# Kernel optimization log

Hardware: AMD Instinct MI355X
Metric: run time of the kernel (lower is better)

Reference implementation:

```python
import jax, jax.numpy as jnp
import numpy as np

D_MODEL = 1024
D_STATE = 16
EXPAND = 2
D_INNER = D_MODEL * EXPAND
BATCH = 512
SEQ = 100
DT = 0.01


def setup_inputs() -> dict:
    key = jax.random.key(0)
    ks = jax.random.split(key, 12)
    s = 0.02
    log_ts = jnp.linspace(jnp.log(0.001), jnp.log(0.1), D_STATE).reshape(1, D_STATE)
    return {
        "x": jax.random.normal(ks[0], (BATCH, SEQ, D_MODEL), jnp.float32),
        "pos_emb": jax.random.normal(ks[1], (1, 100, D_MODEL), jnp.float32),
        "W_in": jax.random.normal(ks[2], (D_INNER, D_MODEL), jnp.float32) * s,
        "b_in": jnp.zeros((D_INNER,), jnp.float32),
        "W_gate": jax.random.normal(ks[3], (D_INNER, D_MODEL), jnp.float32) * s,
        "b_gate": jnp.zeros((D_INNER,), jnp.float32),
        "A_log": log_ts.astype(jnp.float32),
        "W_B": jax.random.normal(ks[4], (D_STATE, D_INNER), jnp.float32) * s,
        "b_B": jnp.zeros((D_STATE,), jnp.float32),
        "W_C": jax.random.normal(ks[5], (D_STATE, D_MODEL), jnp.float32) * s,
        "b_C": jnp.zeros((D_STATE,), jnp.float32),
        "W_out": jax.random.normal(ks[6], (D_MODEL, D_INNER), jnp.float32) * s,
        "b_out": jnp.zeros((D_MODEL,), jnp.float32),
    }


def reference(x, pos_emb, W_in, b_in, W_gate, b_gate, A_log, W_B, b_B, W_C, b_C, W_out, b_out):
    b, s, _ = x.shape
    d_inner = W_in.shape[0]
    d_state = A_log.shape[-1]
    x = x + pos_emb[:, :s, :]
    x_proj = jnp.einsum("bsd,id->bsi", x, W_in) + b_in
    gate = jax.nn.sigmoid(jnp.einsum("bsd,id->bsi", x, W_gate) + b_gate)
    x_gated = x_proj * gate
    B = jnp.einsum("bsi,ni->bsn", x_gated, W_B) + b_B   # (b, s, d_state)
    C = jnp.einsum("bsd,nd->bsn", x, W_C) + b_C         # (b, s, d_state)
    A = jnp.exp(DT * jnp.exp(A_log))                      # (1, d_state), broadcasts over batch

    def step(h, bc):
        Bt, Ct = bc
        h = A * h + Bt
        return h, h * Ct

    h0 = jnp.zeros((b, d_state), x.dtype)
    _, ys = jax.lax.scan(step, h0, (jnp.swapaxes(B, 0, 1), jnp.swapaxes(C, 0, 1)))
    y = jnp.swapaxes(ys, 0, 1)                            # (b, s, d_state)
    d_slice = min(d_state, d_inner)
    expanded = jnp.pad(y[:, :, :d_slice], ((0, 0), (0, 0), (0, d_inner - d_slice)))
    return jnp.einsum("bsi,di->bsd", expanded, W_out) + b_out
```

## Files before the change

### kernel.cpp

```cpp
#include <hip/hip_runtime.h>
#include <hip/hip_bf16.h>
#include <stdint.h>

typedef unsigned short u16;
typedef u16   u16x8 __attribute__((ext_vector_type(8)));
typedef short s16x8 __attribute__((ext_vector_type(8)));
typedef float f32x4 __attribute__((ext_vector_type(4)));

#define TOKENS 51200
#define DMODEL 1024
#define DINNER 2048
#define NSTATE 16
#define SEQLEN 100

#define OFF_XP    0ull
#define OFF_WCAT  104857600ull
#define OFF_WB    113246208ull
#define OFF_WC    113311744ull
#define OFF_BPART 113344512ull
#define OFF_BFIN  165773312ull
#define OFF_CBUF  169050112ull
#define OFF_Y     172326912ull

__device__ __forceinline__ u16 f2b(float f) {
  uint32_t u = __float_as_uint(f);
  uint32_t r = (u + 0x7fffu + ((u >> 16) & 1u)) >> 16;
  return (u16)r;
}
__device__ __forceinline__ float b2f(u16 u) {
  return __uint_as_float(((uint32_t)u) << 16);
}

#define GLL(gp, lp) __builtin_amdgcn_global_load_lds( \
    (__attribute__((address_space(1))) unsigned int*)(gp), \
    (__attribute__((address_space(3))) unsigned int*)(lp), 16, 0, 0)
#define SB0() __builtin_amdgcn_sched_barrier(0)

__global__ void k_prep_x(const float* __restrict__ x, const float* __restrict__ pos,
                         u16* __restrict__ xp) {
  long e = ((long)blockIdx.x * blockDim.x + threadIdx.x) * 8;
  int d = (int)(e & (DMODEL - 1));
  long tok = e >> 10;
  int s = (int)(tok % SEQLEN);
  f32x4 a0 = *(const f32x4*)(x + e);
  f32x4 a1 = *(const f32x4*)(x + e + 4);
  f32x4 p0 = *(const f32x4*)(pos + (size_t)s * DMODEL + d);
  f32x4 p1 = *(const f32x4*)(pos + (size_t)s * DMODEL + d + 4);
  u16x8 o;
  o[0] = f2b(a0[0] + p0[0]); o[1] = f2b(a0[1] + p0[1]);
  o[2] = f2b(a0[2] + p0[2]); o[3] = f2b(a0[3] + p0[3]);
  o[4] = f2b(a1[0] + p1[0]); o[5] = f2b(a1[1] + p1[1]);
  o[6] = f2b(a1[2] + p1[2]); o[7] = f2b(a1[3] + p1[3]);
  *(u16x8*)(xp + e) = o;
}

__global__ void k_prep_w(const float* __restrict__ Win, const float* __restrict__ Wg,
                         u16* __restrict__ w2) {
  long e = ((long)blockIdx.x * blockDim.x + threadIdx.x) * 8;
  int r = (int)(e >> 10), c = (int)(e & 1023);
  int srow = ((r >> 5) << 4) + (r & 15);
  const float* src = ((r & 16) ? Wg : Win) + (size_t)srow * DMODEL + c;
  f32x4 a0 = *(const f32x4*)src;
  f32x4 a1 = *(const f32x4*)(src + 4);
  u16x8 o;
  o[0] = f2b(a0[0]); o[1] = f2b(a0[1]); o[2] = f2b(a0[2]); o[3] = f2b(a0[3]);
  o[4] = f2b(a1[0]); o[5] = f2b(a1[1]); o[6] = f2b(a1[2]); o[7] = f2b(a1[3]);
  *(u16x8*)(w2 + e) = o;
}

__global__ void k_prep_wbc(const float* __restrict__ WB, const float* __restrict__ WC,
                           u16* __restrict__ wb, u16* __restrict__ wc) {
  long e = ((long)blockIdx.x * blockDim.x + threadIdx.x) * 8;
  const float* src; u16* dst;
  if (e < 32768) { src = WB + e; dst = wb + e; }
  else           { src = WC + (e - 32768); dst = wc + (e - 32768); }
  f32x4 a0 = *(const f32x4*)src;
  f32x4 a1 = *(const f32x4*)(src + 4);
  u16x8 o;
  o[0] = f2b(a0[0]); o[1] = f2b(a0[1]); o[2] = f2b(a0[2]); o[3] = f2b(a0[3]);
  o[4] = f2b(a1[0]); o[5] = f2b(a1[1]); o[6] = f2b(a1[2]); o[7] = f2b(a1[3]);
  *(u16x8*)(dst) = o;
}

__global__ __launch_bounds__(512, 2) void k_gemm256(
    const u16* __restrict__ XP, const u16* __restrict__ W2, const u16* __restrict__ WBb,
    const float* __restrict__ b_in, const float* __restrict__ b_gate,
    float* __restrict__ Bpart) {
  extern __shared__ __align__(16) u16 smem[];
  char* smemc = (char*)smem;

  const int tid = threadIdx.x;
  const int bid = blockIdx.x;
  const int nb = ((bid & 7) << 1) | ((bid >> 3) & 1);
  const int rb = bid >> 4;
  const int m0 = rb << 8;
  const int n0 = nb << 8;

  const int arow  = tid >> 3;
  const int acolsw = ((tid & 7) ^ (arow & 7)) << 3;
  const u16* gA = XP + (size_t)(m0 + arow) * DMODEL + acolsw;
  const u16* gB = W2 + (size_t)(n0 + arow) * DMODEL + acolsw;
  const int ldst = tid << 3;

  const int wid = tid >> 6, lane = tid & 63;
  const int wm = wid >> 2, wn = wid & 3;
  const int l15 = lane & 15, lhi = lane >> 4;
  const int swz = (l15 & 7) << 4;
  const int arow0 = (wm << 7) + l15;
  const int brow0 = (wn << 6) + l15;

  auto rdA = [&](int bufb, int m, int ks) -> s16x8 {
    return *(const s16x8*)(smemc + bufb + ((arow0 + (m << 4)) << 7) +
                           (((ks << 6) + (lhi << 4)) ^ swz));
  };
  auto rdB = [&](int bufb, int n, int ks) -> s16x8 {
    return *(const s16x8*)(smemc + bufb + 32768 + ((brow0 + (n << 4)) << 7) +
                           (((ks << 6) + (lhi << 4)) ^ swz));
  };
  auto stgA = [&](int t, int i) {
    const int bb = (t & 1) << 15;
    const size_t go = (size_t)t << 6;
    GLL(gA + go + ((size_t)(2 * i)     << 16), smem + bb + ((2 * i)     << 12) + ldst);
    GLL(gA + go + ((size_t)(2 * i + 1) << 16), smem + bb + ((2 * i + 1) << 12) + ldst);
  };
  auto stgB = [&](int t, int i) {
    const int bb = (t & 1) << 15;
    const size_t go = (size_t)t << 6;
    GLL(gB + go + ((size_t)(2 * i)     << 16), smem + bb + 16384 + ((2 * i)     << 12) + ldst);
    GLL(gB + go + ((size_t)(2 * i + 1) << 16), smem + bb + 16384 + ((2 * i + 1) << 12) + ldst);
  };

  f32x4 acc[8][4] = {};

  stgA(0, 0); stgA(0, 1); stgB(0, 0); stgB(0, 1);
  stgA(1, 0); stgA(1, 1); stgB(1, 0); stgB(1, 1);

#pragma unroll 1
  for (int t = 0; t < 16; ++t) {
    if (t == 15) asm volatile("s_waitcnt vmcnt(0)" ::: "memory");
    else         asm volatile("s_waitcnt vmcnt(8)" ::: "memory");
    SB0();
    asm volatile("s_barrier" ::: "memory");
    SB0();
    const int bufb = (t & 1) << 16;

    s16x8 afl[4][2], afh[4][2], bfr[4][2];
#pragma unroll
    for (int m = 0; m < 4; ++m) { afl[m][0] = rdA(bufb, m, 0); afl[m][1] = rdA(bufb, m, 1); }
#pragma unroll
    for (int n = 0; n < 2; ++n) { bfr[n][0] = rdB(bufb, n, 0); bfr[n][1] = rdB(bufb, n, 1); }
    __builtin_amdgcn_s_setprio(1);
#pragma unroll
    for (int ks = 0; ks < 2; ++ks)
#pragma unroll
      for (int m = 0; m < 4; ++m)
#pragma unroll
        for (int n = 0; n < 2; ++n)
          acc[m][n] = __builtin_amdgcn_mfma_f32_16x16x32_bf16(afl[m][ks], bfr[n][ks], acc[m][n], 0, 0, 0);
    __builtin_amdgcn_s_setprio(0);

#pragma unroll
    for (int n = 2; n < 4; ++n) { bfr[n][0] = rdB(bufb, n, 0); bfr[n][1] = rdB(bufb, n, 1); }
    __builtin_amdgcn_s_setprio(1);
#pragma unroll
    for (int ks = 0; ks < 2; ++ks)
#pragma unroll
      for (int m = 0; m < 4; ++m)
#pragma unroll
        for (int n = 0; n < 2; ++n)
          acc[m][n + 2] = __builtin_amdgcn_mfma_f32_16x16x32_bf16(afl[m][ks], bfr[n + 2][ks], acc[m][n + 2], 0, 0, 0);
    __builtin_amdgcn_s_setprio(0);

#pragma unroll
    for (int m = 0; m < 4; ++m) { afh[m][0] = rdA(bufb, m + 4, 0); afh[m][1] = rdA(bufb, m + 4, 1); }
    asm volatile("s_waitcnt lgkmcnt(0)" ::: "memory");
    SB0();
    asm volatile("s_barrier" ::: "memory");
    SB0();

    if (t < 14) stgA(t + 2, 0);
    SB0();
    __builtin_amdgcn_s_setprio(1);
#pragma unroll
    for (int ks = 0; ks < 2; ++ks)
#pragma unroll
      for (int m = 0; m < 4; ++m)
#pragma unroll
        for (int n = 0; n < 2; ++n)
          acc[m + 4][n + 2] = __builtin_amdgcn_mfma_f32_16x16x32_bf16(afh[m][ks], bfr[n + 2][ks], acc[m + 4][n + 2], 0, 0, 0);
    __builtin_amdgcn_s_setprio(0);
    SB0();
    if (t < 14) stgA(t + 2, 1);
    SB0();
    __builtin_amdgcn_s_setprio(1);
#pragma unroll
    for (int m = 0; m < 4; ++m)
#pragma unroll
      for (int n = 0; n < 2; ++n)
        acc[m + 4][n] = __builtin_amdgcn_mfma_f32_16x16x32_bf16(afh[m][0], bfr[n][0], acc[m + 4][n], 0, 0, 0);
    __builtin_amdgcn_s_setprio(0);
    SB0();
    if (t < 14) stgB(t + 2, 0);
    SB0();
    __builtin_amdgcn_s_setprio(1);
#pragma unroll
    for (int m = 0; m < 4; ++m)
#pragma unroll
      for (int n = 0; n < 2; ++n)
        acc[m + 4][n] = __builtin_amdgcn_mfma_f32_16x16x32_bf16(afh[m][1], bfr[n][1], acc[m + 4][n], 0, 0, 0);
    __builtin_amdgcn_s_setprio(0);
    SB0();
    if (t < 14) stgB(t + 2, 1);
    SB0();
  }

  asm volatile("s_waitcnt lgkmcnt(0)" ::: "memory");
  SB0();
  asm volatile("s_barrier" ::: "memory");
  SB0();

  u16* xg = smem;
  float bi[2], bg[2];
#pragma unroll
  for (int u = 0; u < 2; ++u) {
    const int gcol = (nb << 7) + (((wn << 1) + u) << 4) + l15;
    bi[u] = b_in[gcol];
    bg[u] = b_gate[gcol];
  }
#pragma unroll
  for (int m = 0; m < 8; ++m)
#pragma unroll
    for (int u = 0; u < 2; ++u)
#pragma unroll
      for (int j = 0; j < 4; ++j) {
        const int row = (wm << 7) + (m << 4) + (lhi << 2) + j;
        const int col = (((wn << 1) + u) << 4) + l15;
        float pv = acc[m][2 * u][j] + bi[u];
        float gv = acc[m][2 * u + 1][j] + bg[u];
        xg[row * 136 + col] = f2b(pv / (1.0f + __expf(-gv)));
      }
  asm volatile("s_waitcnt lgkmcnt(0)" ::: "memory");
  asm volatile("s_barrier" ::: "memory");

  f32x4 bacc[2] = {};
#pragma unroll
  for (int m2 = 0; m2 < 2; ++m2)
#pragma unroll
    for (int kc = 0; kc < 4; ++kc) {
      s16x8 av = *(const s16x8*)(xg + ((wid << 5) + (m2 << 4) + l15) * 136 + (kc << 5) + (lhi << 3));
      s16x8 bv = *(const s16x8*)(WBb + (size_t)l15 * DINNER + (nb << 7) + (kc << 5) + (lhi << 3));
      bacc[m2] = __builtin_amdgcn_mfma_f32_16x16x32_bf16(av, bv, bacc[m2], 0, 0, 0);
    }
#pragma unroll
  for (int m2 = 0; m2 < 2; ++m2) {
    float* outp = Bpart + ((size_t)nb * TOKENS + m0 + (wid << 5) + (m2 << 4) + (lhi << 2)) * NSTATE + l15;
#pragma unroll
    for (int j = 0; j < 4; ++j) outp[j * NSTATE] = bacc[m2][j];
  }
}

__global__ __launch_bounds__(256) void k_C(const u16* __restrict__ XP, const u16* __restrict__ WC,
                                           const float* __restrict__ bC, float* __restrict__ Cb) {
  __shared__ __align__(16) u16 wcl[16 * 1032];
  const int tid = threadIdx.x;
  const int m0 = blockIdx.x << 6;
#pragma unroll
  for (int i = 0; i < 8; ++i) {
    int c = i * 256 + tid;
    int row = c >> 7, col = c & 127;
    *(u16x8*)(wcl + row * 1032 + (col << 3)) = *(const u16x8*)(WC + (row << 10) + (col << 3));
  }
  __syncthreads();
  const int wv = tid >> 6, lane = tid & 63;
  const int l15 = lane & 15, lhi = lane >> 4;
  const u16* xr = XP + (size_t)(m0 + (wv << 4) + l15) * DMODEL + (lhi << 3);
  const u16* wr = wcl + l15 * 1032 + (lhi << 3);
  f32x4 acc = {};
#pragma unroll
  for (int t = 0; t < 32; ++t) {
    s16x8 av = *(const s16x8*)(xr + t * 32);
    s16x8 bv = *(const s16x8*)(wr + t * 32);
    acc = __builtin_amdgcn_mfma_f32_16x16x32_bf16(av, bv, acc, 0, 0, 0);
  }
  const float bc = bC[l15];
  float* o = Cb + (size_t)(m0 + (wv << 4) + (lhi << 2)) * NSTATE + l15;
#pragma unroll
  for (int j = 0; j < 4; ++j) o[j * NSTATE] = acc[j] + bc;
}

__global__ void k_finB(const float* __restrict__ Bpart, const float* __restrict__ bB,
                       float* __restrict__ Bf) {
  const long i = (long)blockIdx.x * blockDim.x + threadIdx.x;
  f32x4 s = {};
#pragma unroll
  for (int cb = 0; cb < 16; ++cb)
    s += *(const f32x4*)(Bpart + (size_t)cb * (TOKENS * NSTATE) + i * 4);
  s += *(const f32x4*)(bB + ((i & 3) << 2));
  *(f32x4*)(Bf + i * 4) = s;
}

__global__ void k_scan(const float* __restrict__ Bf, const float* __restrict__ Cb,
                       const float* __restrict__ Alog, float* __restrict__ Y) {
  const int t = threadIdx.x;
  const int b = blockIdx.x * 16 + (t >> 4);
  const int n = t & 15;
  const float A = __expf(0.01f * __expf(Alog[n]));
  float h = 0.f;
  const size_t base = (size_t)b * SEQLEN * NSTATE + n;
  for (int s = 0; s < SEQLEN; ++s) {
    const size_t idx = base + (size_t)s * NSTATE;
    h = A * h + Bf[idx];
    Y[idx] = h * Cb[idx];
  }
}

__global__ __launch_bounds__(256) void k_out(const float* __restrict__ Y,
                                             const float* __restrict__ Wout,
                                             const float* __restrict__ bout,
                                             float* __restrict__ out) {
  __shared__ float ys[32][16];
  const int tid = threadIdx.x;
  const long t0 = (long)blockIdx.x * 32;
  for (int i = tid; i < 512; i += 256) ys[i >> 4][i & 15] = Y[t0 * 16 + i];
  const int d0 = tid << 2;
  float w[4][16];
#pragma unroll
  for (int j = 0; j < 4; ++j)
#pragma unroll
    for (int q = 0; q < 4; ++q) {
      f32x4 wv = *(const f32x4*)(Wout + (size_t)(d0 + j) * DINNER + q * 4);
#pragma unroll
      for (int e = 0; e < 4; ++e) w[j][q * 4 + e] = wv[e];
    }
  f32x4 bo = *(const f32x4*)(bout + d0);
  __syncthreads();
  for (int r = 0; r < 32; ++r) {
    f32x4 acc = bo;
#pragma unroll
    for (int n = 0; n < 16; ++n) {
      const float yv = ys[r][n];
      acc[0] += yv * w[0][n];
      acc[1] += yv * w[1][n];
      acc[2] += yv * w[2][n];
      acc[3] += yv * w[3][n];
    }
    *(f32x4*)(out + (t0 + r) * 1024 + d0) = acc;
  }
}

extern "C" void kernel_launch(void* const* d_in, const int* in_sizes, int n_in,
                              void* d_out, int out_size, void* d_ws, size_t ws_size,
                              hipStream_t stream) {
  const float* x    = (const float*)d_in[0];
  const float* pos  = (const float*)d_in[1];
  const float* Win  = (const float*)d_in[2];
  const float* bin  = (const float*)d_in[3];
  const float* Wg   = (const float*)d_in[4];
  const float* bg   = (const float*)d_in[5];
  const float* Alog = (const float*)d_in[6];
  const float* WB   = (const float*)d_in[7];
  const float* bB   = (const float*)d_in[8];
  const float* WC   = (const float*)d_in[9];
  const float* bC   = (const float*)d_in[10];
  const float* Wout = (const float*)d_in[11];
  const float* bout = (const float*)d_in[12];

  char* ws = (char*)d_ws;
  u16*   XP   = (u16*)(ws + OFF_XP);
  u16*   W2   = (u16*)(ws + OFF_WCAT);
  u16*   WBb  = (u16*)(ws + OFF_WB);
  u16*   WCb  = (u16*)(ws + OFF_WC);
  float* BP   = (float*)(ws + OFF_BPART);
  float* BF   = (float*)(ws + OFF_BFIN);
  float* CB   = (float*)(ws + OFF_CBUF);
  float* Yb   = (float*)(ws + OFF_Y);

  hipFuncSetAttribute((const void*)k_gemm256,
                      hipFuncAttributeMaxDynamicSharedMemorySize, 131072);

  k_prep_x  <<<25600, 256, 0, stream>>>(x, pos, XP);
  k_prep_w  <<<2048, 256, 0, stream>>>(Win, Wg, W2);
  k_prep_wbc<<<24, 256, 0, stream>>>(WB, WC, WBb, WCb);
  k_gemm256 <<<3200, 512, 131072, stream>>>(XP, W2, WBb, bin, bg, BP);
  k_C       <<<800, 256, 0, stream>>>(XP, WCb, bC, CB);
  k_finB    <<<800, 256, 0, stream>>>(BP, bB, BF);
  k_scan    <<<32, 256, 0, stream>>>(BF, CB, Alog, Yb);
  k_out     <<<1600, 256, 0, stream>>>(Yb, Wout, bout, (float*)d_out);
}
```

Before: 565.3 us.

## Split GEMM K tile into half-K LDS subtiles with finer four-phase load/MFMA schedule

Restructures the main bf16 GEMM mainloop so each 64-wide K tile is stored in LDS as two 32-wide halves per matrix, with a new XOR swizzle for 64-byte rows. The loop becomes four phases, each loading fragments, issuing one quarter of the global-to-LDS loads, and running 16 MFMAs, separated by extra barriers. The aim is to spread global loads more evenly across compute and to cut LDS bank conflicts and register pressure from fragment buffers. The cost is more barriers per iteration and a changed prefetch distance, with the B second half of the next tile issued one stage later.

```diff
diff --git a/kernel.cpp b/kernel.cpp
--- a/kernel.cpp
+++ b/kernel.cpp
@@ -96,121 +96,121 @@
   const int m0 = rb << 8;
   const int n0 = nb << 8;
 
-  const int arow  = tid >> 3;
-  const int acolsw = ((tid & 7) ^ (arow & 7)) << 3;
-  const u16* gA = XP + (size_t)(m0 + arow) * DMODEL + acolsw;
-  const u16* gB = W2 + (size_t)(n0 + arow) * DMODEL + acolsw;
+  const int srow = tid >> 2;
+  const int csrc = ((tid & 3) ^ ((tid >> 3) & 3)) << 3;
+  const u16* gA = XP + (size_t)(m0 + srow) * DMODEL + csrc;
+  const u16* gB = W2 + (size_t)(n0 + srow) * DMODEL + csrc;
   const int ldst = tid << 3;
 
   const int wid = tid >> 6, lane = tid & 63;
   const int wm = wid >> 2, wn = wid & 3;
   const int l15 = lane & 15, lhi = lane >> 4;
-  const int swz = (l15 & 7) << 4;
-  const int arow0 = (wm << 7) + l15;
-  const int brow0 = (wn << 6) + l15;
-
-  auto rdA = [&](int bufb, int m, int ks) -> s16x8 {
-    return *(const s16x8*)(smemc + bufb + ((arow0 + (m << 4)) << 7) +
-                           (((ks << 6) + (lhi << 4)) ^ swz));
+  const int kch = (lhi ^ ((l15 >> 1) & 3)) << 4;
+
+  auto rdA = [&](int bufb, int ks, int m) -> s16x8 {
+    const int rr = (wm << 7) + (m << 4) + l15;
+    return *(const s16x8*)(smemc + bufb + (ks << 14) + (rr << 6) + kch);
   };
-  auto rdB = [&](int bufb, int n, int ks) -> s16x8 {
-    return *(const s16x8*)(smemc + bufb + 32768 + ((brow0 + (n << 4)) << 7) +
-                           (((ks << 6) + (lhi << 4)) ^ swz));
+  auto rdB = [&](int bufb, int ks, int n) -> s16x8 {
+    const int rr = (wn << 6) + (n << 4) + l15;
+    return *(const s16x8*)(smemc + bufb + 32768 + (ks << 14) + (rr << 6) + kch);
   };
-  auto stgA = [&](int t, int i) {
-    const int bb = (t & 1) << 15;
-    const size_t go = (size_t)t << 6;
-    GLL(gA + go + ((size_t)(2 * i)     << 16), smem + bb + ((2 * i)     << 12) + ldst);
-    GLL(gA + go + ((size_t)(2 * i + 1) << 16), smem + bb + ((2 * i + 1) << 12) + ldst);
+  auto STG = [&](int mat, int kh, int t) {
+    const int bu = ((t & 1) << 15) + (mat << 14) + (kh << 13);
+    const u16* g = (mat ? gB : gA) + ((size_t)t << 6) + (kh << 5);
+    GLL(g,          smem + bu + ldst);
+    GLL(g + 131072, smem + bu + 4096 + ldst);
   };
-  auto stgB = [&](int t, int i) {
-    const int bb = (t & 1) << 15;
-    const size_t go = (size_t)t << 6;
-    GLL(gB + go + ((size_t)(2 * i)     << 16), smem + bb + 16384 + ((2 * i)     << 12) + ldst);
-    GLL(gB + go + ((size_t)(2 * i + 1) << 16), smem + bb + 16384 + ((2 * i + 1) << 12) + ldst);
-  };
 
   f32x4 acc[8][4] = {};
 
-  stgA(0, 0); stgA(0, 1); stgB(0, 0); stgB(0, 1);
-  stgA(1, 0); stgA(1, 1); stgB(1, 0); stgB(1, 1);
+  STG(0, 0, 0); STG(1, 0, 0); STG(0, 1, 0); STG(1, 1, 0);
+  STG(0, 0, 1); STG(1, 0, 1); STG(0, 1, 1);
 
 #pragma unroll 1
   for (int t = 0; t < 16; ++t) {
     if (t == 15) asm volatile("s_waitcnt vmcnt(0)" ::: "memory");
-    else         asm volatile("s_waitcnt vmcnt(8)" ::: "memory");
+    else         asm volatile("s_waitcnt vmcnt(6)" ::: "memory");
     SB0();
     asm volatile("s_barrier" ::: "memory");
     SB0();
     const int bufb = (t & 1) << 16;
-
-    s16x8 afl[4][2], afh[4][2], bfr[4][2];
-#pragma unroll
-    for (int m = 0; m < 4; ++m) { afl[m][0] = rdA(bufb, m, 0); afl[m][1] = rdA(bufb, m, 1); }
-#pragma unroll
-    for (int n = 0; n < 2; ++n) { bfr[n][0] = rdB(bufb, n, 0); bfr[n][1] = rdB(bufb, n, 1); }
+    s16x8 a0[8], a1[8], bl[2], bh[2];
+
+#pragma unroll
+    for (int m = 0; m < 8; ++m) a0[m] = rdA(bufb, 0, m);
+#pragma unroll
+    for (int n = 0; n < 2; ++n) bl[n] = rdB(bufb, 0, n);
+    if (t < 15) STG(1, 1, t + 1);
+    SB0();
+    asm volatile("s_barrier" ::: "memory");
+    asm volatile("s_waitcnt lgkmcnt(0)" ::: "memory");
+    SB0();
     __builtin_amdgcn_s_setprio(1);
 #pragma unroll
-    for (int ks = 0; ks < 2; ++ks)
-#pragma unroll
-      for (int m = 0; m < 4; ++m)
-#pragma unroll
-        for (int n = 0; n < 2; ++n)
-          acc[m][n] = __builtin_amdgcn_mfma_f32_16x16x32_bf16(afl[m][ks], bfr[n][ks], acc[m][n], 0, 0, 0);
+    for (int m = 0; m < 8; ++m)
+#pragma unroll
+      for (int n = 0; n < 2; ++n)
+        acc[m][n] = __builtin_amdgcn_mfma_f32_16x16x32_bf16(a0[m], bl[n], acc[m][n], 0, 0, 0);
     __builtin_amdgcn_s_setprio(0);
-
-#pragma unroll
-    for (int n = 2; n < 4; ++n) { bfr[n][0] = rdB(bufb, n, 0); bfr[n][1] = rdB(bufb, n, 1); }
+    SB0();
+    asm volatile("s_barrier" ::: "memory");
+    SB0();
+
+#pragma unroll
+    for (int n = 0; n < 2; ++n) bh[n] = rdB(bufb, 0, n + 2);
+    if (t < 14) STG(0, 0, t + 2);
+    SB0();
+    asm volatile("s_barrier" ::: "memory");
+    asm volatile("s_waitcnt lgkmcnt(0)" ::: "memory");
+    SB0();
     __builtin_amdgcn_s_setprio(1);
 #pragma unroll
-    for (int ks = 0; ks < 2; ++ks)
-#pragma unroll
-      for (int m = 0; m < 4; ++m)
-#pragma unroll
-        for (int n = 0; n < 2; ++n)
-          acc[m][n + 2] = __builtin_amdgcn_mfma_f32_16x16x32_bf16(afl[m][ks], bfr[n + 2][ks], acc[m][n + 2], 0, 0, 0);
+    for (int m = 0; m < 8; ++m)
+#pragma unroll
+      for (int n = 0; n < 2; ++n)
+        acc[m][n + 2] = __builtin_amdgcn_mfma_f32_16x16x32_bf16(a0[m], bh[n], acc[m][n + 2], 0, 0, 0);
     __builtin_amdgcn_s_setprio(0);
-
-#pragma unroll
-    for (int m = 0; m < 4; ++m) { afh[m][0] = rdA(bufb, m + 4, 0); afh[m][1] = rdA(bufb, m + 4, 1); }
+    SB0();
+    asm volatile("s_barrier" ::: "memory");
+    SB0();
+
+#pragma unroll
+    for (int m = 0; m < 8; ++m) a1[m] = rdA(bufb, 1, m);
+#pragma unroll
+    for (int n = 0; n < 2; ++n) bl[n] = rdB(bufb, 1, n);
+    if (t < 14) STG(1, 0, t + 2);
+    SB0();
+    asm volatile("s_barrier" ::: "memory");
     asm volatile("s_waitcnt lgkmcnt(0)" ::: "memory");
     SB0();
-    asm volatile("s_barrier" ::: "memory");
-    SB0();
-
-    if (t < 14) stgA(t + 2, 0);
-    SB0();
     __builtin_amdgcn_s_setprio(1);
 #pragma unroll
-    for (int ks = 0; ks < 2; ++ks)
-#pragma unroll
-      for (int m = 0; m < 4; ++m)
-#pragma unroll
-        for (int n = 0; n < 2; ++n)
-          acc[m + 4][n + 2] = __builtin_amdgcn_mfma_f32_16x16x32_bf16(afh[m][ks], bfr[n + 2][ks], acc[m + 4][n + 2], 0, 0, 0);
+    for (int m = 0; m < 8; ++m)
+#pragma unroll
+      for (int n = 0; n < 2; ++n)
+        acc[m][n] = __builtin_amdgcn_mfma_f32_16x16x32_bf16(a1[m], bl[n], acc[m][n], 0, 0, 0);
     __builtin_amdgcn_s_setprio(0);
     SB0();
-    if (t < 14) stgA(t + 2, 1);
+    asm volatile("s_barrier" ::: "memory");
+    SB0();
+
+#pragma unroll
+    for (int n = 0; n < 2; ++n) bh[n] = rdB(bufb, 1, n + 2);
+    if (t < 14) STG(0, 1, t + 2);
+    SB0();
+    asm volatile("s_barrier" ::: "memory");
+    asm volatile("s_waitcnt lgkmcnt(0)" ::: "memory");
     SB0();
     __builtin_amdgcn_s_setprio(1);
 #pragma unroll
-    for (int m = 0; m < 4; ++m)
+    for (int m = 0; m < 8; ++m)
 #pragma unroll
       for (int n = 0; n < 2; ++n)
-        acc[m + 4][n] = __builtin_amdgcn_mfma_f32_16x16x32_bf16(afh[m][0], bfr[n][0], acc[m + 4][n], 0, 0, 0);
+        acc[m][n + 2] = __builtin_amdgcn_mfma_f32_16x16x32_bf16(a1[m], bh[n], acc[m][n + 2], 0, 0, 0);
     __builtin_amdgcn_s_setprio(0);
     SB0();
-    if (t < 14) stgB(t + 2, 0);
-    SB0();
-    __builtin_amdgcn_s_setprio(1);
-#pragma unroll
-    for (int m = 0; m < 4; ++m)
-#pragma unroll
-      for (int n = 0; n < 2; ++n)
-        acc[m + 4][n] = __builtin_amdgcn_mfma_f32_16x16x32_bf16(afh[m][1], bfr[n][1], acc[m + 4][n], 0, 0, 0);
-    __builtin_amdgcn_s_setprio(0);
-    SB0();
-    if (t < 14) stgB(t + 2, 1);
+    asm volatile("s_barrier" ::: "memory");
     SB0();
   }
 
```

Result: slower. 605.8 us (+7.1%).
